# Kernel tuning notes

Measured on AMD Instinct MI355X. Metric: run time of the kernel, lower is better.

## Reference

```python
import jax, jax.numpy as jnp
import numpy as np

B, TD, TE, H = 8, 128, 256, 512


def setup_inputs() -> dict:
    key = jax.random.key(0)
    k1, k2, k3, k4, k5, k6 = jax.random.split(key, 6)
    enc = jax.random.normal(k1, (B, TE, H), dtype=jnp.float32)
    dec = jax.random.normal(k2, (B, TD, H), dtype=jnp.float32)
    mask = jax.random.randint(k3, (B, TE), 0, 2).astype(jnp.bool_)
    # glorot-ish scale for weights
    W1 = jax.random.normal(k4, (H, H), dtype=jnp.float32) * (1.0 / np.sqrt(H))
    W2 = jax.random.normal(k5, (H, H), dtype=jnp.float32) * (1.0 / np.sqrt(H))
    V = jax.random.normal(k6, (H, 1), dtype=jnp.float32) * (1.0 / np.sqrt(H))
    return {"encoder_outputs": enc, "decoder_outputs": dec,
            "encoder_mask": mask, "W1": W1, "W2": W2, "V": V}


def reference(encoder_outputs, decoder_outputs, encoder_mask, W1, W2, V):
    # Bahdanau additive attention.
    # enc: [B, Te, H], dec: [B, Td, H], mask: [B, Te]
    ew = jnp.einsum('bsh,hk->bsk', encoder_outputs, W1)   # [B, Te, H]
    dw = jnp.einsum('bth,hk->btk', decoder_outputs, W2)   # [B, Td, H]
    # broadcast add -> [B, Td, Te, H] (the large intermediate)
    s = jnp.tanh(ew[:, None, :, :] + dw[:, :, None, :])
    score = jnp.einsum('btsh,h->bts', s, V[:, 0])          # [B, Td, Te]
    m = encoder_mask.astype(jnp.float32)                   # [B, Te]
    score = score + (1.0 - m)[:, None, :] * (-1e9)
    attention_weights = jax.nn.softmax(score, axis=2)      # [B, Td, Te]
    context_vector = jnp.einsum('bts,bsh->bth', attention_weights, encoder_outputs)
    return context_vector, attention_weights
```

## Files before the change

kernel.cpp:

```cpp
#include <hip/hip_runtime.h>
#include <hip/hip_bf16.h>
#include <math.h>

constexpr int kB  = 8;
constexpr int kTD = 128;
constexpr int kTE = 256;
constexpr int kH  = 512;

constexpr float kTwoLog2e = 2.8853900817779268f;
constexpr float kLog2e    = 1.4426950408889634f;

constexpr int TM = 4;
constexpr int GEMM_BLOCKS = 384;

typedef __attribute__((ext_vector_type(8)))  short short8;
typedef __attribute__((ext_vector_type(16))) float f32x16;

__device__ __forceinline__ unsigned short f2bf(float x) {
    unsigned int u = __float_as_uint(x);
    return (unsigned short)((u + 0x7fffu + ((u >> 16) & 1u)) >> 16);
}
__device__ __forceinline__ float bf2f(unsigned short h) {
    return __uint_as_float(((unsigned int)h) << 16);
}

__global__ __launch_bounds__(256)
void prep_kernel(const float* __restrict__ enc, const float* __restrict__ dec,
                 const float* __restrict__ W1, const float* __restrict__ W2,
                 const void* __restrict__ mask_raw,
                 float* __restrict__ ewt, float* __restrict__ dwc,
                 float* __restrict__ mask_f) {
    const int bx = blockIdx.x;
    const int tid = threadIdx.x;

    if (bx == GEMM_BLOCKS) {
        const unsigned int* w = (const unsigned int*)mask_raw;
        unsigned int gt1 = 0, flt = 0;
        for (int i = tid; i < 512; i += 256) {
            unsigned int v = w[i];
            if (v == 0x3f800000u) flt = 1;
            else if (v > 1u) gt1 = 1;
        }
        __shared__ unsigned int s_gt1, s_flt;
        if (tid == 0) { s_gt1 = 0u; s_flt = 0u; }
        __syncthreads();
        if (gt1) atomicOr(&s_gt1, 1u);
        if (flt) atomicOr(&s_flt, 1u);
        __syncthreads();
        const int mode = s_flt ? 2 : (s_gt1 ? 1 : 0);
        for (int i = tid; i < kB * kTE; i += 256) {
            float val;
            if (mode == 2)      val = ((const float*)mask_raw)[i];
            else if (mode == 1) val = (float)(((const unsigned char*)mask_raw)[i]);
            else                val = (float)(((const int*)mask_raw)[i]);
            mask_f[i] = val;
        }
        return;
    }

    const int mt = bx >> 3;
    const int nt = bx & 7;
    const bool is_enc = (mt < 32);
    const int m0 = mt * 64;
    const int n0 = nt * 64;
    const float* Abase = is_enc ? (enc + (size_t)m0 * kH)
                                : (dec + (size_t)(m0 - 2048) * kH);
    const float* W = is_enc ? W1 : W2;

    __shared__ __align__(16) unsigned short Ahi[64][40], Alo[64][40];
    __shared__ __align__(16) unsigned short Bhi[64][40], Blo[64][40];
    __shared__ float Ws[32][68];

    const int lane = tid & 63;
    const int wv   = tid >> 6;
    const int wr   = wv >> 1, wc = wv & 1;
    const int col  = lane & 31, hi5 = lane >> 5;

    const int ar  = tid >> 2;
    const int akc = (tid & 3) * 8;
    const int wkr = tid >> 3;
    const int wnc = (tid & 7) * 8;
    const int pn  = tid & 63;
    const int pkc = (tid >> 6) * 8;

    f32x16 acc = {};

    float4 a0p = *(const float4*)&Abase[(size_t)ar * kH + akc];
    float4 a1p = *(const float4*)&Abase[(size_t)ar * kH + akc + 4];
    float4 w0p = *(const float4*)&W[(size_t)wkr * kH + n0 + wnc];
    float4 w1p = *(const float4*)&W[(size_t)wkr * kH + n0 + wnc + 4];

    for (int step = 0; step < 16; ++step) {
        *(float4*)&Ws[wkr][wnc]     = w0p;
        *(float4*)&Ws[wkr][wnc + 4] = w1p;
        {
            uint4 H, L;
            float f[8] = {a0p.x, a0p.y, a0p.z, a0p.w, a1p.x, a1p.y, a1p.z, a1p.w};
            unsigned short hs[8], ls[8];
            #pragma unroll
            for (int j = 0; j < 8; ++j) {
                hs[j] = f2bf(f[j]);
                ls[j] = f2bf(f[j] - bf2f(hs[j]));
            }
            H.x = hs[0] | (hs[1] << 16); H.y = hs[2] | (hs[3] << 16);
            H.z = hs[4] | (hs[5] << 16); H.w = hs[6] | (hs[7] << 16);
            L.x = ls[0] | (ls[1] << 16); L.y = ls[2] | (ls[3] << 16);
            L.z = ls[4] | (ls[5] << 16); L.w = ls[6] | (ls[7] << 16);
            *(uint4*)&Ahi[ar][akc] = H;
            *(uint4*)&Alo[ar][akc] = L;
        }
        __syncthreads();

        {
            uint4 H, L;
            unsigned short hs[8], ls[8];
            #pragma unroll
            for (int j = 0; j < 8; ++j) {
                float x = Ws[pkc + j][pn];
                hs[j] = f2bf(x);
                ls[j] = f2bf(x - bf2f(hs[j]));
            }
            H.x = hs[0] | (hs[1] << 16); H.y = hs[2] | (hs[3] << 16);
            H.z = hs[4] | (hs[5] << 16); H.w = hs[6] | (hs[7] << 16);
            L.x = ls[0] | (ls[1] << 16); L.y = ls[2] | (ls[3] << 16);
            L.z = ls[4] | (ls[5] << 16); L.w = ls[6] | (ls[7] << 16);
            *(uint4*)&Bhi[pn][pkc] = H;
            *(uint4*)&Blo[pn][pkc] = L;
        }

        if (step < 15) {
            const int k1 = (step + 1) * 32;
            a0p = *(const float4*)&Abase[(size_t)ar * kH + k1 + akc];
            a1p = *(const float4*)&Abase[(size_t)ar * kH + k1 + akc + 4];
            w0p = *(const float4*)&W[(size_t)(k1 + wkr) * kH + n0 + wnc];
            w1p = *(const float4*)&W[(size_t)(k1 + wkr) * kH + n0 + wnc + 4];
        }
        __syncthreads();

        #pragma unroll
        for (int kc = 0; kc < 32; kc += 16) {
            const int ka = kc + hi5 * 8;
            short8 ah = *(const short8*)&Ahi[wr * 32 + col][ka];
            short8 al = *(const short8*)&Alo[wr * 32 + col][ka];
            short8 bh = *(const short8*)&Bhi[wc * 32 + col][ka];
            short8 bl = *(const short8*)&Blo[wc * 32 + col][ka];
            acc = __builtin_amdgcn_mfma_f32_32x32x16_bf16(ah, bh, acc, 0, 0, 0);
            acc = __builtin_amdgcn_mfma_f32_32x32x16_bf16(ah, bl, acc, 0, 0, 0);
            acc = __builtin_amdgcn_mfma_f32_32x32x16_bf16(al, bh, acc, 0, 0, 0);
        }
        __syncthreads();
    }

    const int h = n0 + wc * 32 + col;
    if (is_enc) {
        #pragma unroll
        for (int reg = 0; reg < 16; ++reg) {
            const int row = (reg & 3) + 8 * (reg >> 2) + 4 * hi5;
            const int gm = m0 + wr * 32 + row;
            const int bb = gm >> 8, sE = gm & 255;
            float val = __builtin_amdgcn_exp2f(acc[reg] * kTwoLog2e);
            ewt[(((size_t)bb * 128 + (h >> 2)) * 256 + sE) * 4 + (h & 3)] = val;
        }
    } else {
        #pragma unroll
        for (int reg = 0; reg < 16; ++reg) {
            const int row = (reg & 3) + 8 * (reg >> 2) + 4 * hi5;
            const int dm = (m0 - 2048) + wr * 32 + row;
            float val = __builtin_amdgcn_exp2f(acc[reg] * kTwoLog2e);
            dwc[(size_t)dm * kH + h] = val;
        }
    }
}

__global__ __launch_bounds__(1024)
void fused_attn_kernel(const float* __restrict__ ewt, const float* __restrict__ dwc,
                       const float* __restrict__ enc, const float* __restrict__ V,
                       const float* __restrict__ mask_f,
                       float* __restrict__ ctx_out, float* __restrict__ attn_out) {
    const int bid = blockIdx.x;
    const int b   = bid & 7;
    const int t0  = (bid >> 3) * TM;
    const int tid = threadIdx.x;
    const int s   = tid & 255;
    const int hq  = tid >> 8;
    const int hqu = __builtin_amdgcn_readfirstlane(hq);

    __shared__ float part[3 * TM * kTE];
    __shared__ float4 wgt4[kTE];
    __shared__ float red_mx[4][TM], red_sm[4][TM];

    const float4* E4 = (const float4*)ewt + ((size_t)(b * 128 + hqu * 32) * 256 + s);
    const float4* Pb = (const float4*)(dwc + (size_t)(b * kTD + t0) * kH) + hqu * 32;
    const float4* V4 = (const float4*)V + hqu * 32;

    float a0 = 0.0f, a1 = 0.0f, a2 = 0.0f, a3 = 0.0f;
    #pragma unroll 2
    for (int g = 0; g < 32; ++g) {
        float4 e  = E4[(size_t)g * 256];
        float4 vv = V4[g];
        {   float4 q = Pb[g];
            float A_ = fmaf(e.x, q.x, 1.0f), B_ = fmaf(e.y, q.y, 1.0f);
            float C_ = fmaf(e.z, q.z, 1.0f), D_ = fmaf(e.w, q.w, 1.0f);
            float t1 = fmaf(vv.y, A_, vv.x * B_);
            float t2 = fmaf(vv.w, C_, vv.z * D_);
            float AB = A_ * B_, CD = C_ * D_;
            float num = fmaf(t2, AB, t1 * CD);
            a0 = fmaf(num, __builtin_amdgcn_rcpf(AB * CD), a0); }
        {   float4 q = Pb[128 + g];
            float A_ = fmaf(e.x, q.x, 1.0f), B_ = fmaf(e.y, q.y, 1.0f);
            float C_ = fmaf(e.z, q.z, 1.0f), D_ = fmaf(e.w, q.w, 1.0f);
            float t1 = fmaf(vv.y, A_, vv.x * B_);
            float t2 = fmaf(vv.w, C_, vv.z * D_);
            float AB = A_ * B_, CD = C_ * D_;
            float num = fmaf(t2, AB, t1 * CD);
            a1 = fmaf(num, __builtin_amdgcn_rcpf(AB * CD), a1); }
        {   float4 q = Pb[256 + g];
            float A_ = fmaf(e.x, q.x, 1.0f), B_ = fmaf(e.y, q.y, 1.0f);
            float C_ = fmaf(e.z, q.z, 1.0f), D_ = fmaf(e.w, q.w, 1.0f);
            float t1 = fmaf(vv.y, A_, vv.x * B_);
            float t2 = fmaf(vv.w, C_, vv.z * D_);
            float AB = A_ * B_, CD = C_ * D_;
            float num = fmaf(t2, AB, t1 * CD);
            a2 = fmaf(num, __builtin_amdgcn_rcpf(AB * CD), a2); }
        {   float4 q = Pb[384 + g];
            float A_ = fmaf(e.x, q.x, 1.0f), B_ = fmaf(e.y, q.y, 1.0f);
            float C_ = fmaf(e.z, q.z, 1.0f), D_ = fmaf(e.w, q.w, 1.0f);
            float t1 = fmaf(vv.y, A_, vv.x * B_);
            float t2 = fmaf(vv.w, C_, vv.z * D_);
            float AB = A_ * B_, CD = C_ * D_;
            float num = fmaf(t2, AB, t1 * CD);
            a3 = fmaf(num, __builtin_amdgcn_rcpf(AB * CD), a3); }
    }

    if (hq > 0) {
        float* pp = &part[(hq - 1) * TM * kTE];
        pp[0 * kTE + s] = a0; pp[1 * kTE + s] = a1;
        pp[2 * kTE + s] = a2; pp[3 * kTE + s] = a3;
    }
    __syncthreads();

    const bool active = (hq == 0);
    const int wv = s >> 6;
    float sc0, sc1, sc2, sc3;
    if (active) {
        const float pen = (1.0f - mask_f[b * kTE + s]) * -1e9f;
        sc0 = -2.0f * ((a0 + part[0 * TM * kTE + 0 * kTE + s]) +
                       (part[1 * TM * kTE + 0 * kTE + s] + part[2 * TM * kTE + 0 * kTE + s])) + pen;
        sc1 = -2.0f * ((a1 + part[0 * TM * kTE + 1 * kTE + s]) +
                       (part[1 * TM * kTE + 1 * kTE + s] + part[2 * TM * kTE + 1 * kTE + s])) + pen;
        sc2 = -2.0f * ((a2 + part[0 * TM * kTE + 2 * kTE + s]) +
                       (part[1 * TM * kTE + 2 * kTE + s] + part[2 * TM * kTE + 2 * kTE + s])) + pen;
        sc3 = -2.0f * ((a3 + part[0 * TM * kTE + 3 * kTE + s]) +
                       (part[1 * TM * kTE + 3 * kTE + s] + part[2 * TM * kTE + 3 * kTE + s])) + pen;
        float m0 = sc0, m1 = sc1, m2 = sc2, m3 = sc3;
        #pragma unroll
        for (int off = 1; off < 64; off <<= 1) {
            m0 = fmaxf(m0, __shfl_xor(m0, off));
            m1 = fmaxf(m1, __shfl_xor(m1, off));
            m2 = fmaxf(m2, __shfl_xor(m2, off));
            m3 = fmaxf(m3, __shfl_xor(m3, off));
        }
        if ((s & 63) == 0) {
            red_mx[wv][0] = m0; red_mx[wv][1] = m1;
            red_mx[wv][2] = m2; red_mx[wv][3] = m3;
        }
    }
    __syncthreads();

    float p0, p1, p2, p3;
    if (active) {
        float m0 = fmaxf(fmaxf(red_mx[0][0], red_mx[1][0]), fmaxf(red_mx[2][0], red_mx[3][0]));
        float m1 = fmaxf(fmaxf(red_mx[0][1], red_mx[1][1]), fmaxf(red_mx[2][1], red_mx[3][1]));
        float m2 = fmaxf(fmaxf(red_mx[0][2], red_mx[1][2]), fmaxf(red_mx[2][2], red_mx[3][2]));
        float m3 = fmaxf(fmaxf(red_mx[0][3], red_mx[1][3]), fmaxf(red_mx[2][3], red_mx[3][3]));
        p0 = __builtin_amdgcn_exp2f((sc0 - m0) * kLog2e);
        p1 = __builtin_amdgcn_exp2f((sc1 - m1) * kLog2e);
        p2 = __builtin_amdgcn_exp2f((sc2 - m2) * kLog2e);
        p3 = __builtin_amdgcn_exp2f((sc3 - m3) * kLog2e);
        float s0 = p0, s1 = p1, s2 = p2, s3 = p3;
        #pragma unroll
        for (int off = 1; off < 64; off <<= 1) {
            s0 += __shfl_xor(s0, off);
            s1 += __shfl_xor(s1, off);
            s2 += __shfl_xor(s2, off);
            s3 += __shfl_xor(s3, off);
        }
        if ((s & 63) == 0) {
            red_sm[wv][0] = s0; red_sm[wv][1] = s1;
            red_sm[wv][2] = s2; red_sm[wv][3] = s3;
        }
    }
    __syncthreads();

    if (active) {
        float s0 = (red_sm[0][0] + red_sm[1][0]) + (red_sm[2][0] + red_sm[3][0]);
        float s1 = (red_sm[0][1] + red_sm[1][1]) + (red_sm[2][1] + red_sm[3][1]);
        float s2 = (red_sm[0][2] + red_sm[1][2]) + (red_sm[2][2] + red_sm[3][2]);
        float s3 = (red_sm[0][3] + red_sm[1][3]) + (red_sm[2][3] + red_sm[3][3]);
        float4 w;
        w.x = p0 * __builtin_amdgcn_rcpf(s0);
        w.y = p1 * __builtin_amdgcn_rcpf(s1);
        w.z = p2 * __builtin_amdgcn_rcpf(s2);
        w.w = p3 * __builtin_amdgcn_rcpf(s3);
        wgt4[s] = w;
        float* ao = attn_out + (size_t)(b * kTD + t0) * kTE + s;
        ao[0]       = w.x;
        ao[kTE]     = w.y;
        ao[2 * kTE] = w.z;
        ao[3 * kTE] = w.w;
    }
    __syncthreads();

    const int sh = tid >> 9;
    const int h  = tid & 511;
    const float* encb = enc + (size_t)b * kTE * kH + (size_t)sh * 128 * kH + h;
    float c0 = 0.0f, c1 = 0.0f, c2 = 0.0f, c3 = 0.0f;
    #pragma unroll 4
    for (int ss = 0; ss < 128; ++ss) {
        float e = encb[(size_t)ss * kH];
        float4 w = wgt4[sh * 128 + ss];
        c0 = fmaf(w.x, e, c0);
        c1 = fmaf(w.y, e, c1);
        c2 = fmaf(w.z, e, c2);
        c3 = fmaf(w.w, e, c3);
    }
    float* pctx = part;
    if (sh == 1) {
        pctx[0 * 512 + h] = c0; pctx[1 * 512 + h] = c1;
        pctx[2 * 512 + h] = c2; pctx[3 * 512 + h] = c3;
    }
    __syncthreads();
    if (sh == 0) {
        float* co = ctx_out + (size_t)(b * kTD + t0) * kH + h;
        co[0]       = c0 + pctx[0 * 512 + h];
        co[kH]      = c1 + pctx[1 * 512 + h];
        co[2 * kH]  = c2 + pctx[2 * 512 + h];
        co[3 * kH]  = c3 + pctx[3 * 512 + h];
    }
}

extern "C" void kernel_launch(void* const* d_in, const int* in_sizes, int n_in,
                              void* d_out, int out_size, void* d_ws, size_t ws_size,
                              hipStream_t stream) {
    const float* enc  = (const float*)d_in[0];
    const float* dec  = (const float*)d_in[1];
    const void*  mask = d_in[2];
    const float* W1   = (const float*)d_in[3];
    const float* W2   = (const float*)d_in[4];
    const float* V    = (const float*)d_in[5];

    float* ctx_out  = (float*)d_out;
    float* attn_out = (float*)d_out + kB * kTD * kH;

    char* ws = (char*)d_ws;
    float* mask_f = (float*)ws;
    float* ewt    = (float*)(ws + 8192);
    float* dwc    = (float*)(ws + 8192 + (size_t)kB * kTE * kH * 4);

    hipLaunchKernelGGL(prep_kernel, dim3(GEMM_BLOCKS + 1), dim3(256), 0, stream,
                       enc, dec, W1, W2, mask, ewt, dwc, mask_f);
    hipLaunchKernelGGL(fused_attn_kernel, dim3(kB * kTD / TM), dim3(1024), 0, stream,
                       ewt, dwc, enc, V, mask_f, ctx_out, attn_out);
}
```

Before: 46.82 us.

## Fuse projection GEMM and attention into one cooperative kernel with grid sync

```diff
diff --git a/kernel.cpp b/kernel.cpp
--- a/kernel.cpp
+++ b/kernel.cpp
@@ -1,6 +1,9 @@
 #include <hip/hip_runtime.h>
+#include <hip/hip_cooperative_groups.h>
 #include <hip/hip_bf16.h>
 #include <math.h>
+
+namespace cg = cooperative_groups;
 
 constexpr int kB  = 8;
 constexpr int kTD = 128;
@@ -11,7 +14,6 @@
 constexpr float kLog2e    = 1.4426950408889634f;
 
 constexpr int TM = 4;
-constexpr int GEMM_BLOCKS = 384;
 
 typedef __attribute__((ext_vector_type(8)))  short short8;
 typedef __attribute__((ext_vector_type(16))) float f32x16;
@@ -24,177 +26,182 @@
     return __uint_as_float(((unsigned int)h) << 16);
 }
 
-__global__ __launch_bounds__(256)
-void prep_kernel(const float* __restrict__ enc, const float* __restrict__ dec,
+struct SmemA {
+    unsigned short Ahi[4][64][40];
+    unsigned short Alo[4][64][40];
+    unsigned short Bhi[64][40];
+    unsigned short Blo[64][40];
+    float Ws[32][68];
+};
+struct SmemB {
+    float  part[3 * TM * kTE];
+    float4 wgt4[kTE];
+    float  red_mx[4][TM];
+    float  red_sm[4][TM];
+    float4 pctx[4][TM][128];
+};
+
+__global__ __launch_bounds__(1024, 4)
+void mega_kernel(const float* __restrict__ enc, const float* __restrict__ dec,
                  const float* __restrict__ W1, const float* __restrict__ W2,
-                 const void* __restrict__ mask_raw,
+                 const void* __restrict__ mask_raw, const float* __restrict__ V,
                  float* __restrict__ ewt, float* __restrict__ dwc,
-                 float* __restrict__ mask_f) {
-    const int bx = blockIdx.x;
+                 float* __restrict__ mask_f,
+                 float* __restrict__ ctx_out, float* __restrict__ attn_out) {
+    __shared__ __align__(16) union { SmemA a; SmemB b; } smem;
+    __shared__ unsigned int s_gt1, s_flt;
+
+    const int bx  = blockIdx.x;
     const int tid = threadIdx.x;
 
-    if (bx == GEMM_BLOCKS) {
+    if (bx < 96) {
+        const bool is_enc = (bx < 64);
+        const int base = is_enc ? bx : bx - 64;
+        const int mq = base >> 3;
+        const int nt = base & 7;
+        const int n0 = nt * 64;
+        const int g   = tid >> 8;
+        const int lid = tid & 255;
+        const int mt  = mq * 4 + g;
+        const float* Abase = is_enc ? (enc + (size_t)mt * 64 * kH)
+                                    : (dec + (size_t)mt * 64 * kH);
+        const float* W = is_enc ? W1 : W2;
+
+        const int ar  = lid >> 2;
+        const int akc = (lid & 3) * 8;
+        const int wkr = tid >> 4;
+        const int wnc = (tid & 15) * 4;
+        const int pn  = tid >> 2;
+        const int pkc = (tid & 3) * 8;
+
+        const int lane = tid & 63;
+        const int gw   = (tid >> 6) & 3;
+        const int wr   = gw >> 1, wc = gw & 1;
+        const int col  = lane & 31, hi5 = lane >> 5;
+
+        f32x16 acc = {};
+        const float* Arow = Abase + (size_t)ar * kH;
+
+        float4 a0p = *(const float4*)&Arow[akc];
+        float4 a1p = *(const float4*)&Arow[akc + 4];
+        float4 w0p = {};
+        if (tid < 512) w0p = *(const float4*)&W[(size_t)wkr * kH + n0 + wnc];
+
+        for (int step = 0; step < 16; ++step) {
+            if (tid < 512) *(float4*)&smem.a.Ws[wkr][wnc] = w0p;
+            {
+                uint4 H, L;
+                float f[8] = {a0p.x, a0p.y, a0p.z, a0p.w, a1p.x, a1p.y, a1p.z, a1p.w};
+                unsigned short hs[8], ls[8];
+                #pragma unroll
+                for (int j = 0; j < 8; ++j) {
+                    hs[j] = f2bf(f[j]);
+                    ls[j] = f2bf(f[j] - bf2f(hs[j]));
+                }
+                H.x = hs[0] | (hs[1] << 16); H.y = hs[2] | (hs[3] << 16);
+                H.z = hs[4] | (hs[5] << 16); H.w = hs[6] | (hs[7] << 16);
+                L.x = ls[0] | (ls[1] << 16); L.y = ls[2] | (ls[3] << 16);
+                L.z = ls[4] | (ls[5] << 16); L.w = ls[6] | (ls[7] << 16);
+                *(uint4*)&smem.a.Ahi[g][ar][akc] = H;
+                *(uint4*)&smem.a.Alo[g][ar][akc] = L;
+            }
+            __syncthreads();
+
+            if (tid < 256) {
+                uint4 H, L;
+                unsigned short hs[8], ls[8];
+                #pragma unroll
+                for (int j = 0; j < 8; ++j) {
+                    float x = smem.a.Ws[pkc + j][pn];
+                    hs[j] = f2bf(x);
+                    ls[j] = f2bf(x - bf2f(hs[j]));
+                }
+                H.x = hs[0] | (hs[1] << 16); H.y = hs[2] | (hs[3] << 16);
+                H.z = hs[4] | (hs[5] << 16); H.w = hs[6] | (hs[7] << 16);
+                L.x = ls[0] | (ls[1] << 16); L.y = ls[2] | (ls[3] << 16);
+                L.z = ls[4] | (ls[5] << 16); L.w = ls[6] | (ls[7] << 16);
+                *(uint4*)&smem.a.Bhi[pn][pkc] = H;
+                *(uint4*)&smem.a.Blo[pn][pkc] = L;
+            }
+            if (step < 15) {
+                const int k1 = (step + 1) * 32;
+                a0p = *(const float4*)&Arow[k1 + akc];
+                a1p = *(const float4*)&Arow[k1 + akc + 4];
+                if (tid < 512)
+                    w0p = *(const float4*)&W[(size_t)(k1 + wkr) * kH + n0 + wnc];
+            }
+            __syncthreads();
+
+            #pragma unroll
+            for (int kc = 0; kc < 32; kc += 16) {
+                const int ka = kc + hi5 * 8;
+                short8 ah = *(const short8*)&smem.a.Ahi[g][wr * 32 + col][ka];
+                short8 al = *(const short8*)&smem.a.Alo[g][wr * 32 + col][ka];
+                short8 bh = *(const short8*)&smem.a.Bhi[wc * 32 + col][ka];
+                short8 bl = *(const short8*)&smem.a.Blo[wc * 32 + col][ka];
+                acc = __builtin_amdgcn_mfma_f32_32x32x16_bf16(ah, bh, acc, 0, 0, 0);
+                acc = __builtin_amdgcn_mfma_f32_32x32x16_bf16(ah, bl, acc, 0, 0, 0);
+                acc = __builtin_amdgcn_mfma_f32_32x32x16_bf16(al, bh, acc, 0, 0, 0);
+            }
+            __syncthreads();
+        }
+
+        const int h = n0 + wc * 32 + col;
+        if (is_enc) {
+            #pragma unroll
+            for (int reg = 0; reg < 16; ++reg) {
+                const int row = (reg & 3) + 8 * (reg >> 2) + 4 * hi5;
+                const int gm = mt * 64 + wr * 32 + row;
+                const int bb = gm >> 8, sE = gm & 255;
+                float val = __builtin_amdgcn_exp2f(acc[reg] * kTwoLog2e);
+                ewt[(((size_t)bb * 128 + (h >> 2)) * 256 + sE) * 4 + (h & 3)] = val;
+            }
+        } else {
+            #pragma unroll
+            for (int reg = 0; reg < 16; ++reg) {
+                const int row = (reg & 3) + 8 * (reg >> 2) + 4 * hi5;
+                const int dm = mt * 64 + wr * 32 + row;
+                float val = __builtin_amdgcn_exp2f(acc[reg] * kTwoLog2e);
+                dwc[(size_t)dm * kH + h] = val;
+            }
+        }
+    } else if (bx == 96) {
         const unsigned int* w = (const unsigned int*)mask_raw;
         unsigned int gt1 = 0, flt = 0;
-        for (int i = tid; i < 512; i += 256) {
-            unsigned int v = w[i];
+        if (tid < 512) {
+            unsigned int v = w[tid];
             if (v == 0x3f800000u) flt = 1;
             else if (v > 1u) gt1 = 1;
         }
-        __shared__ unsigned int s_gt1, s_flt;
         if (tid == 0) { s_gt1 = 0u; s_flt = 0u; }
         __syncthreads();
         if (gt1) atomicOr(&s_gt1, 1u);
         if (flt) atomicOr(&s_flt, 1u);
         __syncthreads();
         const int mode = s_flt ? 2 : (s_gt1 ? 1 : 0);
-        for (int i = tid; i < kB * kTE; i += 256) {
+        for (int i = tid; i < kB * kTE; i += 1024) {
             float val;
             if (mode == 2)      val = ((const float*)mask_raw)[i];
             else if (mode == 1) val = (float)(((const unsigned char*)mask_raw)[i]);
             else                val = (float)(((const int*)mask_raw)[i]);
             mask_f[i] = val;
         }
-        return;
-    }
-
-    const int mt = bx >> 3;
-    const int nt = bx & 7;
-    const bool is_enc = (mt < 32);
-    const int m0 = mt * 64;
-    const int n0 = nt * 64;
-    const float* Abase = is_enc ? (enc + (size_t)m0 * kH)
-                                : (dec + (size_t)(m0 - 2048) * kH);
-    const float* W = is_enc ? W1 : W2;
-
-    __shared__ __align__(16) unsigned short Ahi[64][40], Alo[64][40];
-    __shared__ __align__(16) unsigned short Bhi[64][40], Blo[64][40];
-    __shared__ float Ws[32][68];
-
-    const int lane = tid & 63;
-    const int wv   = tid >> 6;
-    const int wr   = wv >> 1, wc = wv & 1;
-    const int col  = lane & 31, hi5 = lane >> 5;
-
-    const int ar  = tid >> 2;
-    const int akc = (tid & 3) * 8;
-    const int wkr = tid >> 3;
-    const int wnc = (tid & 7) * 8;
-    const int pn  = tid & 63;
-    const int pkc = (tid >> 6) * 8;
-
-    f32x16 acc = {};
-
-    float4 a0p = *(const float4*)&Abase[(size_t)ar * kH + akc];
-    float4 a1p = *(const float4*)&Abase[(size_t)ar * kH + akc + 4];
-    float4 w0p = *(const float4*)&W[(size_t)wkr * kH + n0 + wnc];
-    float4 w1p = *(const float4*)&W[(size_t)wkr * kH + n0 + wnc + 4];
-
-    for (int step = 0; step < 16; ++step) {
-        *(float4*)&Ws[wkr][wnc]     = w0p;
-        *(float4*)&Ws[wkr][wnc + 4] = w1p;
-        {
-            uint4 H, L;
-            float f[8] = {a0p.x, a0p.y, a0p.z, a0p.w, a1p.x, a1p.y, a1p.z, a1p.w};
-            unsigned short hs[8], ls[8];
-            #pragma unroll
-            for (int j = 0; j < 8; ++j) {
-                hs[j] = f2bf(f[j]);
-                ls[j] = f2bf(f[j] - bf2f(hs[j]));
-            }
-            H.x = hs[0] | (hs[1] << 16); H.y = hs[2] | (hs[3] << 16);
-            H.z = hs[4] | (hs[5] << 16); H.w = hs[6] | (hs[7] << 16);
-            L.x = ls[0] | (ls[1] << 16); L.y = ls[2] | (ls[3] << 16);
-            L.z = ls[4] | (ls[5] << 16); L.w = ls[6] | (ls[7] << 16);
-            *(uint4*)&Ahi[ar][akc] = H;
-            *(uint4*)&Alo[ar][akc] = L;
-        }
-        __syncthreads();
-
-        {
-            uint4 H, L;
-            unsigned short hs[8], ls[8];
-            #pragma unroll
-            for (int j = 0; j < 8; ++j) {
-                float x = Ws[pkc + j][pn];
-                hs[j] = f2bf(x);
-                ls[j] = f2bf(x - bf2f(hs[j]));
-            }
-            H.x = hs[0] | (hs[1] << 16); H.y = hs[2] | (hs[3] << 16);
-            H.z = hs[4] | (hs[5] << 16); H.w = hs[6] | (hs[7] << 16);
-            L.x = ls[0] | (ls[1] << 16); L.y = ls[2] | (ls[3] << 16);
-            L.z = ls[4] | (ls[5] << 16); L.w = ls[6] | (ls[7] << 16);
-            *(uint4*)&Bhi[pn][pkc] = H;
-            *(uint4*)&Blo[pn][pkc] = L;
-        }
-
-        if (step < 15) {
-            const int k1 = (step + 1) * 32;
-            a0p = *(const float4*)&Abase[(size_t)ar * kH + k1 + akc];
-            a1p = *(const float4*)&Abase[(size_t)ar * kH + k1 + akc + 4];
-            w0p = *(const float4*)&W[(size_t)(k1 + wkr) * kH + n0 + wnc];
-            w1p = *(const float4*)&W[(size_t)(k1 + wkr) * kH + n0 + wnc + 4];
-        }
-        __syncthreads();
-
-        #pragma unroll
-        for (int kc = 0; kc < 32; kc += 16) {
-            const int ka = kc + hi5 * 8;
-            short8 ah = *(const short8*)&Ahi[wr * 32 + col][ka];
-            short8 al = *(const short8*)&Alo[wr * 32 + col][ka];
-            short8 bh = *(const short8*)&Bhi[wc * 32 + col][ka];
-            short8 bl = *(const short8*)&Blo[wc * 32 + col][ka];
-            acc = __builtin_amdgcn_mfma_f32_32x32x16_bf16(ah, bh, acc, 0, 0, 0);
-            acc = __builtin_amdgcn_mfma_f32_32x32x16_bf16(ah, bl, acc, 0, 0, 0);
-            acc = __builtin_amdgcn_mfma_f32_32x32x16_bf16(al, bh, acc, 0, 0, 0);
-        }
-        __syncthreads();
-    }
-
-    const int h = n0 + wc * 32 + col;
-    if (is_enc) {
-        #pragma unroll
-        for (int reg = 0; reg < 16; ++reg) {
-            const int row = (reg & 3) + 8 * (reg >> 2) + 4 * hi5;
-            const int gm = m0 + wr * 32 + row;
-            const int bb = gm >> 8, sE = gm & 255;
-            float val = __builtin_amdgcn_exp2f(acc[reg] * kTwoLog2e);
-            ewt[(((size_t)bb * 128 + (h >> 2)) * 256 + sE) * 4 + (h & 3)] = val;
-        }
-    } else {
-        #pragma unroll
-        for (int reg = 0; reg < 16; ++reg) {
-            const int row = (reg & 3) + 8 * (reg >> 2) + 4 * hi5;
-            const int dm = (m0 - 2048) + wr * 32 + row;
-            float val = __builtin_amdgcn_exp2f(acc[reg] * kTwoLog2e);
-            dwc[(size_t)dm * kH + h] = val;
-        }
-    }
-}
-
-__global__ __launch_bounds__(1024)
-void fused_attn_kernel(const float* __restrict__ ewt, const float* __restrict__ dwc,
-                       const float* __restrict__ enc, const float* __restrict__ V,
-                       const float* __restrict__ mask_f,
-                       float* __restrict__ ctx_out, float* __restrict__ attn_out) {
-    const int bid = blockIdx.x;
-    const int b   = bid & 7;
-    const int t0  = (bid >> 3) * TM;
-    const int tid = threadIdx.x;
+    }
+
+    cg::this_grid().sync();
+
+    const int b   = bx & 7;
+    const int t0  = (bx >> 3) * TM;
     const int s   = tid & 255;
     const int hq  = tid >> 8;
     const int hqu = __builtin_amdgcn_readfirstlane(hq);
 
-    __shared__ float part[3 * TM * kTE];
-    __shared__ float4 wgt4[kTE];
-    __shared__ float red_mx[4][TM], red_sm[4][TM];
-
     const float4* E4 = (const float4*)ewt + ((size_t)(b * 128 + hqu * 32) * 256 + s);
     const float4* Pb = (const float4*)(dwc + (size_t)(b * kTD + t0) * kH) + hqu * 32;
     const float4* V4 = (const float4*)V + hqu * 32;
 
     float a0 = 0.0f, a1 = 0.0f, a2 = 0.0f, a3 = 0.0f;
-    #pragma unroll 2
+    #pragma unroll 4
     for (int g = 0; g < 32; ++g) {
         float4 e  = E4[(size_t)g * 256];
         float4 vv = V4[g];
@@ -233,25 +240,26 @@
     }
 
     if (hq > 0) {
-        float* pp = &part[(hq - 1) * TM * kTE];
+        float* pp = &smem.b.part[(hq - 1) * TM * kTE];
         pp[0 * kTE + s] = a0; pp[1 * kTE + s] = a1;
         pp[2 * kTE + s] = a2; pp[3 * kTE + s] = a3;
     }
     __syncthreads();
 
     const bool active = (hq == 0);
-    const int wv = s >> 6;
+    const int wvq = s >> 6;
     float sc0, sc1, sc2, sc3;
     if (active) {
+        const float* P = smem.b.part;
         const float pen = (1.0f - mask_f[b * kTE + s]) * -1e9f;
-        sc0 = -2.0f * ((a0 + part[0 * TM * kTE + 0 * kTE + s]) +
-                       (part[1 * TM * kTE + 0 * kTE + s] + part[2 * TM * kTE + 0 * kTE + s])) + pen;
-        sc1 = -2.0f * ((a1 + part[0 * TM * kTE + 1 * kTE + s]) +
-                       (part[1 * TM * kTE + 1 * kTE + s] + part[2 * TM * kTE + 1 * kTE + s])) + pen;
-        sc2 = -2.0f * ((a2 + part[0 * TM * kTE + 2 * kTE + s]) +
-                       (part[1 * TM * kTE + 2 * kTE + s] + part[2 * TM * kTE + 2 * kTE + s])) + pen;
-        sc3 = -2.0f * ((a3 + part[0 * TM * kTE + 3 * kTE + s]) +
-                       (part[1 * TM * kTE + 3 * kTE + s] + part[2 * TM * kTE + 3 * kTE + s])) + pen;
+        sc0 = -2.0f * ((a0 + P[0 * TM * kTE + 0 * kTE + s]) +
+                       (P[1 * TM * kTE + 0 * kTE + s] + P[2 * TM * kTE + 0 * kTE + s])) + pen;
+        sc1 = -2.0f * ((a1 + P[0 * TM * kTE + 1 * kTE + s]) +
+                       (P[1 * TM * kTE + 1 * kTE + s] + P[2 * TM * kTE + 1 * kTE + s])) + pen;
+        sc2 = -2.0f * ((a2 + P[0 * TM * kTE + 2 * kTE + s]) +
+                       (P[1 * TM * kTE + 2 * kTE + s] + P[2 * TM * kTE + 2 * kTE + s])) + pen;
+        sc3 = -2.0f * ((a3 + P[0 * TM * kTE + 3 * kTE + s]) +
+                       (P[1 * TM * kTE + 3 * kTE + s] + P[2 * TM * kTE + 3 * kTE + s])) + pen;
         float m0 = sc0, m1 = sc1, m2 = sc2, m3 = sc3;
         #pragma unroll
         for (int off = 1; off < 64; off <<= 1) {
@@ -261,18 +269,19 @@
             m3 = fmaxf(m3, __shfl_xor(m3, off));
         }
         if ((s & 63) == 0) {
-            red_mx[wv][0] = m0; red_mx[wv][1] = m1;
-            red_mx[wv][2] = m2; red_mx[wv][3] = m3;
+            smem.b.red_mx[wvq][0] = m0; smem.b.red_mx[wvq][1] = m1;
+            smem.b.red_mx[wvq][2] = m2; smem.b.red_mx[wvq][3] = m3;
         }
     }
     __syncthreads();
 
     float p0, p1, p2, p3;
     if (active) {
-        float m0 = fmaxf(fmaxf(red_mx[0][0], red_mx[1][0]), fmaxf(red_mx[2][0], red_mx[3][0]));
-        float m1 = fmaxf(fmaxf(red_mx[0][1], red_mx[1][1]), fmaxf(red_mx[2][1], red_mx[3][1]));
-        float m2 = fmaxf(fmaxf(red_mx[0][2], red_mx[1][2]), fmaxf(red_mx[2][2], red_mx[3][2]));
-        float m3 = fmaxf(fmaxf(red_mx[0][3], red_mx[1][3]), fmaxf(red_mx[2][3], red_mx[3][3]));
+        const auto& R = smem.b.red_mx;
+        float m0 = fmaxf(fmaxf(R[0][0], R[1][0]), fmaxf(R[2][0], R[3][0]));
+        float m1 = fmaxf(fmaxf(R[0][1], R[1][1]), fmaxf(R[2][1], R[3][1]));
+        float m2 = fmaxf(fmaxf(R[0][2], R[1][2]), fmaxf(R[2][2], R[3][2]));
+        float m3 = fmaxf(fmaxf(R[0][3], R[1][3]), fmaxf(R[2][3], R[3][3]));
         p0 = __builtin_amdgcn_exp2f((sc0 - m0) * kLog2e);
         p1 = __builtin_amdgcn_exp2f((sc1 - m1) * kLog2e);
         p2 = __builtin_amdgcn_exp2f((sc2 - m2) * kLog2e);
@@ -286,23 +295,24 @@
             s3 += __shfl_xor(s3, off);
         }
         if ((s & 63) == 0) {
-            red_sm[wv][0] = s0; red_sm[wv][1] = s1;
-            red_sm[wv][2] = s2; red_sm[wv][3] = s3;
+            smem.b.red_sm[wvq][0] = s0; smem.b.red_sm[wvq][1] = s1;
+            smem.b.red_sm[wvq][2] = s2; smem.b.red_sm[wvq][3] = s3;
         }
     }
     __syncthreads();
 
     if (active) {
-        float s0 = (red_sm[0][0] + red_sm[1][0]) + (red_sm[2][0] + red_sm[3][0]);
-        float s1 = (red_sm[0][1] + red_sm[1][1]) + (red_sm[2][1] + red_sm[3][1]);
-        float s2 = (red_sm[0][2] + red_sm[1][2]) + (red_sm[2][2] + red_sm[3][2]);
-        float s3 = (red_sm[0][3] + red_sm[1][3]) + (red_sm[2][3] + red_sm[3][3]);
+        const auto& R = smem.b.red_sm;
+        float s0 = (R[0][0] + R[1][0]) + (R[2][0] + R[3][0]);
+        float s1 = (R[0][1] + R[1][1]) + (R[2][1] + R[3][1]);
+        float s2 = (R[0][2] + R[1][2]) + (R[2][2] + R[3][2]);
+        float s3 = (R[0][3] + R[1][3]) + (R[2][3] + R[3][3]);
         float4 w;
         w.x = p0 * __builtin_amdgcn_rcpf(s0);
         w.y = p1 * __builtin_amdgcn_rcpf(s1);
         w.z = p2 * __builtin_amdgcn_rcpf(s2);
         w.w = p3 * __builtin_amdgcn_rcpf(s3);
-        wgt4[s] = w;
+        smem.b.wgt4[s] = w;
         float* ao = attn_out + (size_t)(b * kTD + t0) * kTE + s;
         ao[0]       = w.x;
         ao[kTE]     = w.y;
@@ -311,31 +321,56 @@
     }
     __syncthreads();
 
-    const int sh = tid >> 9;
-    const int h  = tid & 511;
-    const float* encb = enc + (size_t)b * kTE * kH + (size_t)sh * 128 * kH + h;
-    float c0 = 0.0f, c1 = 0.0f, c2 = 0.0f, c3 = 0.0f;
+    const int th4 = tid & 127;
+    const int sq  = tid >> 7;
+    const float4* enc4 = (const float4*)(enc + (size_t)b * kTE * kH);
+    float4 c[TM];
+    #pragma unroll
+    for (int t = 0; t < TM; ++t) c[t] = float4{0.f, 0.f, 0.f, 0.f};
     #pragma unroll 4
-    for (int ss = 0; ss < 128; ++ss) {
-        float e = encb[(size_t)ss * kH];
-        float4 w = wgt4[sh * 128 + ss];
-        c0 = fmaf(w.x, e, c0);
-        c1 = fmaf(w.y, e, c1);
-        c2 = fmaf(w.z, e, c2);
-        c3 = fmaf(w.w, e, c3);
-    }
-    float* pctx = part;
-    if (sh == 1) {
-        pctx[0 * 512 + h] = c0; pctx[1 * 512 + h] = c1;
-        pctx[2 * 512 + h] = c2; pctx[3 * 512 + h] = c3;
-    }
-    __syncthreads();
-    if (sh == 0) {
-        float* co = ctx_out + (size_t)(b * kTD + t0) * kH + h;
-        co[0]       = c0 + pctx[0 * 512 + h];
-        co[kH]      = c1 + pctx[1 * 512 + h];
-        co[2 * kH]  = c2 + pctx[2 * 512 + h];
-        co[3 * kH]  = c3 + pctx[3 * 512 + h];
+    for (int i = 0; i < 32; ++i) {
+        const int ss = sq * 32 + i;
+        float4 e = enc4[(size_t)ss * 128 + th4];
+        float4 w = smem.b.wgt4[ss];
+        c[0].x = fmaf(w.x, e.x, c[0].x); c[0].y = fmaf(w.x, e.y, c[0].y);
+        c[0].z = fmaf(w.x, e.z, c[0].z); c[0].w = fmaf(w.x, e.w, c[0].w);
+        c[1].x = fmaf(w.y, e.x, c[1].x); c[1].y = fmaf(w.y, e.y, c[1].y);
+        c[1].z = fmaf(w.y, e.z, c[1].z); c[1].w = fmaf(w.y, e.w, c[1].w);
+        c[2].x = fmaf(w.z, e.x, c[2].x); c[2].y = fmaf(w.z, e.y, c[2].y);
+        c[2].z = fmaf(w.z, e.z, c[2].z); c[2].w = fmaf(w.z, e.w, c[2].w);
+        c[3].x = fmaf(w.w, e.x, c[3].x); c[3].y = fmaf(w.w, e.y, c[3].y);
+        c[3].z = fmaf(w.w, e.z, c[3].z); c[3].w = fmaf(w.w, e.w, c[3].w);
+    }
+    if (sq >= 4) {
+        #pragma unroll
+        for (int t = 0; t < TM; ++t) smem.b.pctx[sq - 4][t][th4] = c[t];
+    }
+    __syncthreads();
+    if (sq < 4) {
+        #pragma unroll
+        for (int t = 0; t < TM; ++t) {
+            float4 p = smem.b.pctx[sq][t][th4];
+            c[t].x += p.x; c[t].y += p.y; c[t].z += p.z; c[t].w += p.w;
+        }
+    }
+    __syncthreads();
+    if (sq >= 1 && sq < 4) {
+        #pragma unroll
+        for (int t = 0; t < TM; ++t) smem.b.pctx[sq - 1][t][th4] = c[t];
+    }
+    __syncthreads();
+    if (sq == 0) {
+        #pragma unroll
+        for (int t = 0; t < TM; ++t) {
+            float4 p0v = smem.b.pctx[0][t][th4];
+            float4 p1v = smem.b.pctx[1][t][th4];
+            float4 p2v = smem.b.pctx[2][t][th4];
+            c[t].x += (p0v.x + p1v.x) + p2v.x;
+            c[t].y += (p0v.y + p1v.y) + p2v.y;
+            c[t].z += (p0v.z + p1v.z) + p2v.z;
+            c[t].w += (p0v.w + p1v.w) + p2v.w;
+            *(float4*)&ctx_out[(size_t)(b * kTD + t0 + t) * kH + th4 * 4] = c[t];
+        }
     }
 }
 
@@ -357,8 +392,9 @@
     float* ewt    = (float*)(ws + 8192);
     float* dwc    = (float*)(ws + 8192 + (size_t)kB * kTE * kH * 4);
 
-    hipLaunchKernelGGL(prep_kernel, dim3(GEMM_BLOCKS + 1), dim3(256), 0, stream,
-                       enc, dec, W1, W2, mask, ewt, dwc, mask_f);
-    hipLaunchKernelGGL(fused_attn_kernel, dim3(kB * kTD / TM), dim3(1024), 0, stream,
-                       ewt, dwc, enc, V, mask_f, ctx_out, attn_out);
+    void* args[] = { (void*)&enc, (void*)&dec, (void*)&W1, (void*)&W2,
+                     (void*)&mask, (void*)&V, (void*)&ewt, (void*)&dwc,
+                     (void*)&mask_f, (void*)&ctx_out, (void*)&attn_out };
+    hipLaunchCooperativeKernel((void*)mega_kernel, dim3(256), dim3(1024),
+                               args, 0, stream);
 }
```

New measurement: 102.2 us. 118% more time.

## Stage decoder rows and V in LDS, prefetch encoder, vectorize context reduction

Applied to the files above, without the earlier changes.

```diff
diff --git a/kernel.cpp b/kernel.cpp
--- a/kernel.cpp
+++ b/kernel.cpp
@@ -183,75 +183,79 @@
     const int tid = threadIdx.x;
     const int s   = tid & 255;
     const int hq  = tid >> 8;
-    const int hqu = __builtin_amdgcn_readfirstlane(hq);
-
-    __shared__ float part[3 * TM * kTE];
+
+    __shared__ float p_s[TM * kH];
+    __shared__ float v_s[kH];
+    __shared__ union {
+        float  part[3 * TM * kTE];
+        float4 pctx[4][TM][128];
+    } u;
     __shared__ float4 wgt4[kTE];
     __shared__ float red_mx[4][TM], red_sm[4][TM];
 
-    const float4* E4 = (const float4*)ewt + ((size_t)(b * 128 + hqu * 32) * 256 + s);
-    const float4* Pb = (const float4*)(dwc + (size_t)(b * kTD + t0) * kH) + hqu * 32;
-    const float4* V4 = (const float4*)V + hqu * 32;
+    if (tid < 512)
+        ((float4*)p_s)[tid] =
+            ((const float4*)(dwc + (size_t)(b * kTD + t0) * kH))[tid];
+    else if (tid < 640)
+        ((float4*)v_s)[tid - 512] = ((const float4*)V)[tid - 512];
+    __syncthreads();
+
+    const float4* E4 = (const float4*)ewt + ((size_t)(b * 128 + hq * 32) * 256 + s);
+    const float4* Pq = (const float4*)p_s;
+    const float4* Vq = (const float4*)v_s;
+    const int gb = hq * 32;
 
     float a0 = 0.0f, a1 = 0.0f, a2 = 0.0f, a3 = 0.0f;
-    #pragma unroll 2
-    for (int g = 0; g < 32; ++g) {
-        float4 e  = E4[(size_t)g * 256];
-        float4 vv = V4[g];
-        {   float4 q = Pb[g];
-            float A_ = fmaf(e.x, q.x, 1.0f), B_ = fmaf(e.y, q.y, 1.0f);
-            float C_ = fmaf(e.z, q.z, 1.0f), D_ = fmaf(e.w, q.w, 1.0f);
-            float t1 = fmaf(vv.y, A_, vv.x * B_);
-            float t2 = fmaf(vv.w, C_, vv.z * D_);
-            float AB = A_ * B_, CD = C_ * D_;
-            float num = fmaf(t2, AB, t1 * CD);
-            a0 = fmaf(num, __builtin_amdgcn_rcpf(AB * CD), a0); }
-        {   float4 q = Pb[128 + g];
-            float A_ = fmaf(e.x, q.x, 1.0f), B_ = fmaf(e.y, q.y, 1.0f);
-            float C_ = fmaf(e.z, q.z, 1.0f), D_ = fmaf(e.w, q.w, 1.0f);
-            float t1 = fmaf(vv.y, A_, vv.x * B_);
-            float t2 = fmaf(vv.w, C_, vv.z * D_);
-            float AB = A_ * B_, CD = C_ * D_;
-            float num = fmaf(t2, AB, t1 * CD);
-            a1 = fmaf(num, __builtin_amdgcn_rcpf(AB * CD), a1); }
-        {   float4 q = Pb[256 + g];
-            float A_ = fmaf(e.x, q.x, 1.0f), B_ = fmaf(e.y, q.y, 1.0f);
-            float C_ = fmaf(e.z, q.z, 1.0f), D_ = fmaf(e.w, q.w, 1.0f);
-            float t1 = fmaf(vv.y, A_, vv.x * B_);
-            float t2 = fmaf(vv.w, C_, vv.z * D_);
-            float AB = A_ * B_, CD = C_ * D_;
-            float num = fmaf(t2, AB, t1 * CD);
-            a2 = fmaf(num, __builtin_amdgcn_rcpf(AB * CD), a2); }
-        {   float4 q = Pb[384 + g];
-            float A_ = fmaf(e.x, q.x, 1.0f), B_ = fmaf(e.y, q.y, 1.0f);
-            float C_ = fmaf(e.z, q.z, 1.0f), D_ = fmaf(e.w, q.w, 1.0f);
-            float t1 = fmaf(vv.y, A_, vv.x * B_);
-            float t2 = fmaf(vv.w, C_, vv.z * D_);
-            float AB = A_ * B_, CD = C_ * D_;
-            float num = fmaf(t2, AB, t1 * CD);
-            a3 = fmaf(num, __builtin_amdgcn_rcpf(AB * CD), a3); }
-    }
+    float4 e0 = E4[0], e1 = E4[256], e2 = E4[512], e3 = E4[768];
+
+#define SCORE_T(eV, gg, qt, accv)                                          \
+    {   float4 q = Pq[(qt) * 128 + gb + (gg)];                             \
+        float A_ = fmaf(eV.x, q.x, 1.0f), B_ = fmaf(eV.y, q.y, 1.0f);      \
+        float C_ = fmaf(eV.z, q.z, 1.0f), D_ = fmaf(eV.w, q.w, 1.0f);      \
+        float t1 = fmaf(vv.y, A_, vv.x * B_);                              \
+        float t2 = fmaf(vv.w, C_, vv.z * D_);                              \
+        float AB = A_ * B_, CD = C_ * D_;                                  \
+        accv = fmaf(fmaf(t2, AB, t1 * CD),                                 \
+                    __builtin_amdgcn_rcpf(AB * CD), accv); }
+#define SCORE_STEP(eV, gg)                                                 \
+    {   float4 vv = Vq[gb + (gg)];                                         \
+        SCORE_T(eV, gg, 0, a0) SCORE_T(eV, gg, 1, a1)                      \
+        SCORE_T(eV, gg, 2, a2) SCORE_T(eV, gg, 3, a3) }
+
+    #pragma unroll
+    for (int g = 0; g < 32; g += 4) {
+        float4 f0 = E4[(size_t)(g + 4) * 256];
+        float4 f1 = E4[(size_t)(g + 5) * 256];
+        float4 f2 = E4[(size_t)(g + 6) * 256];
+        float4 f3 = E4[(size_t)(g + 7) * 256];
+        SCORE_STEP(e0, g)     SCORE_STEP(e1, g + 1)
+        SCORE_STEP(e2, g + 2) SCORE_STEP(e3, g + 3)
+        e0 = f0; e1 = f1; e2 = f2; e3 = f3;
+    }
+#undef SCORE_STEP
+#undef SCORE_T
 
     if (hq > 0) {
-        float* pp = &part[(hq - 1) * TM * kTE];
+        float* pp = &u.part[(hq - 1) * TM * kTE];
         pp[0 * kTE + s] = a0; pp[1 * kTE + s] = a1;
         pp[2 * kTE + s] = a2; pp[3 * kTE + s] = a3;
     }
     __syncthreads();
 
     const bool active = (hq == 0);
-    const int wv = s >> 6;
+    const int wvq = s >> 6;
     float sc0, sc1, sc2, sc3;
     if (active) {
+        const float* P = u.part;
         const float pen = (1.0f - mask_f[b * kTE + s]) * -1e9f;
-        sc0 = -2.0f * ((a0 + part[0 * TM * kTE + 0 * kTE + s]) +
-                       (part[1 * TM * kTE + 0 * kTE + s] + part[2 * TM * kTE + 0 * kTE + s])) + pen;
-        sc1 = -2.0f * ((a1 + part[0 * TM * kTE + 1 * kTE + s]) +
-                       (part[1 * TM * kTE + 1 * kTE + s] + part[2 * TM * kTE + 1 * kTE + s])) + pen;
-        sc2 = -2.0f * ((a2 + part[0 * TM * kTE + 2 * kTE + s]) +
-                       (part[1 * TM * kTE + 2 * kTE + s] + part[2 * TM * kTE + 2 * kTE + s])) + pen;
-        sc3 = -2.0f * ((a3 + part[0 * TM * kTE + 3 * kTE + s]) +
-                       (part[1 * TM * kTE + 3 * kTE + s] + part[2 * TM * kTE + 3 * kTE + s])) + pen;
+        sc0 = -2.0f * ((a0 + P[0 * TM * kTE + 0 * kTE + s]) +
+                       (P[1 * TM * kTE + 0 * kTE + s] + P[2 * TM * kTE + 0 * kTE + s])) + pen;
+        sc1 = -2.0f * ((a1 + P[0 * TM * kTE + 1 * kTE + s]) +
+                       (P[1 * TM * kTE + 1 * kTE + s] + P[2 * TM * kTE + 1 * kTE + s])) + pen;
+        sc2 = -2.0f * ((a2 + P[0 * TM * kTE + 2 * kTE + s]) +
+                       (P[1 * TM * kTE + 2 * kTE + s] + P[2 * TM * kTE + 2 * kTE + s])) + pen;
+        sc3 = -2.0f * ((a3 + P[0 * TM * kTE + 3 * kTE + s]) +
+                       (P[1 * TM * kTE + 3 * kTE + s] + P[2 * TM * kTE + 3 * kTE + s])) + pen;
         float m0 = sc0, m1 = sc1, m2 = sc2, m3 = sc3;
         #pragma unroll
         for (int off = 1; off < 64; off <<= 1) {
@@ -261,8 +265,8 @@
             m3 = fmaxf(m3, __shfl_xor(m3, off));
         }
         if ((s & 63) == 0) {
-            red_mx[wv][0] = m0; red_mx[wv][1] = m1;
-            red_mx[wv][2] = m2; red_mx[wv][3] = m3;
+            red_mx[wvq][0] = m0; red_mx[wvq][1] = m1;
+            red_mx[wvq][2] = m2; red_mx[wvq][3] = m3;
         }
     }
     __syncthreads();
@@ -286,8 +290,8 @@
             s3 += __shfl_xor(s3, off);
         }
         if ((s & 63) == 0) {
-            red_sm[wv][0] = s0; red_sm[wv][1] = s1;
-            red_sm[wv][2] = s2; red_sm[wv][3] = s3;
+            red_sm[wvq][0] = s0; red_sm[wvq][1] = s1;
+            red_sm[wvq][2] = s2; red_sm[wvq][3] = s3;
         }
     }
     __syncthreads();
@@ -311,31 +315,56 @@
     }
     __syncthreads();
 
-    const int sh = tid >> 9;
-    const int h  = tid & 511;
-    const float* encb = enc + (size_t)b * kTE * kH + (size_t)sh * 128 * kH + h;
-    float c0 = 0.0f, c1 = 0.0f, c2 = 0.0f, c3 = 0.0f;
-    #pragma unroll 4
-    for (int ss = 0; ss < 128; ++ss) {
-        float e = encb[(size_t)ss * kH];
-        float4 w = wgt4[sh * 128 + ss];
-        c0 = fmaf(w.x, e, c0);
-        c1 = fmaf(w.y, e, c1);
-        c2 = fmaf(w.z, e, c2);
-        c3 = fmaf(w.w, e, c3);
-    }
-    float* pctx = part;
-    if (sh == 1) {
-        pctx[0 * 512 + h] = c0; pctx[1 * 512 + h] = c1;
-        pctx[2 * 512 + h] = c2; pctx[3 * 512 + h] = c3;
-    }
-    __syncthreads();
-    if (sh == 0) {
-        float* co = ctx_out + (size_t)(b * kTD + t0) * kH + h;
-        co[0]       = c0 + pctx[0 * 512 + h];
-        co[kH]      = c1 + pctx[1 * 512 + h];
-        co[2 * kH]  = c2 + pctx[2 * 512 + h];
-        co[3 * kH]  = c3 + pctx[3 * 512 + h];
+    const int th4 = tid & 127;
+    const int sq  = tid >> 7;
+    const float4* enc4 = (const float4*)(enc + (size_t)b * kTE * kH);
+    float4 c[TM];
+    #pragma unroll
+    for (int t = 0; t < TM; ++t) c[t] = float4{0.f, 0.f, 0.f, 0.f};
+    #pragma unroll 8
+    for (int i = 0; i < 32; ++i) {
+        const int ss = sq * 32 + i;
+        float4 e = enc4[(size_t)ss * 128 + th4];
+        float4 w = wgt4[ss];
+        c[0].x = fmaf(w.x, e.x, c[0].x); c[0].y = fmaf(w.x, e.y, c[0].y);
+        c[0].z = fmaf(w.x, e.z, c[0].z); c[0].w = fmaf(w.x, e.w, c[0].w);
+        c[1].x = fmaf(w.y, e.x, c[1].x); c[1].y = fmaf(w.y, e.y, c[1].y);
+        c[1].z = fmaf(w.y, e.z, c[1].z); c[1].w = fmaf(w.y, e.w, c[1].w);
+        c[2].x = fmaf(w.z, e.x, c[2].x); c[2].y = fmaf(w.z, e.y, c[2].y);
+        c[2].z = fmaf(w.z, e.z, c[2].z); c[2].w = fmaf(w.z, e.w, c[2].w);
+        c[3].x = fmaf(w.w, e.x, c[3].x); c[3].y = fmaf(w.w, e.y, c[3].y);
+        c[3].z = fmaf(w.w, e.z, c[3].z); c[3].w = fmaf(w.w, e.w, c[3].w);
+    }
+    if (sq >= 4) {
+        #pragma unroll
+        for (int t = 0; t < TM; ++t) u.pctx[sq - 4][t][th4] = c[t];
+    }
+    __syncthreads();
+    if (sq < 4) {
+        #pragma unroll
+        for (int t = 0; t < TM; ++t) {
+            float4 p = u.pctx[sq][t][th4];
+            c[t].x += p.x; c[t].y += p.y; c[t].z += p.z; c[t].w += p.w;
+        }
+    }
+    __syncthreads();
+    if (sq >= 1 && sq < 4) {
+        #pragma unroll
+        for (int t = 0; t < TM; ++t) u.pctx[sq - 1][t][th4] = c[t];
+    }
+    __syncthreads();
+    if (sq == 0) {
+        #pragma unroll
+        for (int t = 0; t < TM; ++t) {
+            float4 q0v = u.pctx[0][t][th4];
+            float4 q1v = u.pctx[1][t][th4];
+            float4 q2v = u.pctx[2][t][th4];
+            c[t].x += (q0v.x + q1v.x) + q2v.x;
+            c[t].y += (q0v.y + q1v.y) + q2v.y;
+            c[t].z += (q0v.z + q1v.z) + q2v.z;
+            c[t].w += (q0v.w + q1v.w) + q2v.w;
+            *(float4*)&ctx_out[(size_t)(b * kTD + t0 + t) * kH + th4 * 4] = c[t];
+        }
     }
 }
 
```

Measured after the change: 57.73 us. 23.3% more time.
